# Kernel optimization log

Hardware: AMD Instinct MI355X
Metric: run time of the kernel (lower is better)

## Reference

```python
import jax, jax.numpy as jnp
import numpy as np

B, S, D, E, H, F, L, C = 32768, 5, 512, 256, 4, 2048, 2, 5  # batch, sensors, input_dim, embed_dim, heads, ffn, layers, classes
DH = E // H
EPS = 1e-5


def layer_norm(x, g, b):
    m = jnp.mean(x, axis=-1, keepdims=True)
    v = jnp.mean((x - m) ** 2, axis=-1, keepdims=True)
    return (x - m) * jax.lax.rsqrt(v + EPS) * g + b


def setup_inputs() -> dict:
    key = jax.random.key(0)
    ks = jax.random.split(key, 24)
    n = lambda k, shape: (jax.random.normal(k, shape, dtype=jnp.float32) * 0.02)
    return {
        "x": jax.random.normal(ks[0], (B, S, D), dtype=jnp.float32),
        "sensor_types": jax.random.randint(ks[1], (B, S), 0, 2, dtype=jnp.int32),
        "gps_w": n(ks[2], (E, D)), "gps_b": jnp.zeros((E,), jnp.float32),
        "ang_w": n(ks[3], (E, D)), "ang_b": jnp.zeros((E,), jnp.float32),
        "qkv_w": n(ks[4], (L, 3 * E, E)), "qkv_b": jnp.zeros((L, 3 * E), jnp.float32),
        "attn_ow": n(ks[5], (L, E, E)), "attn_ob": jnp.zeros((L, E), jnp.float32),
        "ln1_g": jnp.ones((L, E), jnp.float32), "ln1_b": jnp.zeros((L, E), jnp.float32),
        "ff1_w": n(ks[6], (L, F, E)), "ff1_b": jnp.zeros((L, F), jnp.float32),
        "ff2_w": n(ks[7], (L, E, F)), "ff2_b": jnp.zeros((L, E), jnp.float32),
        "ln2_g": jnp.ones((L, E), jnp.float32), "ln2_b": jnp.zeros((L, E), jnp.float32),
        "fc1_w": n(ks[8], (128, S * E)), "fc1_b": jnp.zeros((128,), jnp.float32),
        "fc2_w": n(ks[9], (64, 128)), "fc2_b": jnp.zeros((64,), jnp.float32),
        "out_w": n(ks[10], (C, 64)), "out_b": jnp.zeros((C,), jnp.float32),
    }


def reference(x, sensor_types, gps_w, gps_b, ang_w, ang_b, qkv_w, qkv_b,
              attn_ow, attn_ob, ln1_g, ln1_b, ff1_w, ff1_b, ff2_w, ff2_b,
              ln2_g, ln2_b, fc1_w, fc1_b, fc2_w, fc2_b, out_w, out_b):
    # Dual-expert routing: compute both branches, blend by mask (same math as masked scatter)
    is_gps = (sensor_types == 0)[..., None]  # [B,S,1]
    g = jax.nn.relu(jnp.einsum('bsd,ed->bse', x, gps_w) + gps_b)
    a = jax.nn.relu(jnp.einsum('bsd,ed->bse', x, ang_w) + ang_b)
    h = jnp.where(is_gps, g, a)  # [B,S,E]

    # TransformerEncoder (post-LN, ReLU FFN, dropout inactive at eval)
    for l in range(L):
        qkv = jnp.einsum('bse,fe->bsf', h, qkv_w[l]) + qkv_b[l]  # [B,S,3E]
        q, k, v = jnp.split(qkv, 3, axis=-1)
        q = q.reshape(B, S, H, DH); k = k.reshape(B, S, H, DH); v = v.reshape(B, S, H, DH)
        scores = jnp.einsum('bqhd,bkhd->bhqk', q, k) / jnp.sqrt(jnp.float32(DH))
        attn = jax.nn.softmax(scores, axis=-1)
        o = jnp.einsum('bhqk,bkhd->bqhd', attn, v).reshape(B, S, E)
        o = o @ attn_ow[l].T + attn_ob[l]
        h = layer_norm(h + o, ln1_g[l], ln1_b[l])
        ff = jax.nn.relu(h @ ff1_w[l].T + ff1_b[l]) @ ff2_w[l].T + ff2_b[l]
        h = layer_norm(h + ff, ln2_g[l], ln2_b[l])

    z = h.reshape(B, S * E)
    z = z @ fc1_w.T + fc1_b
    z = z @ fc2_w.T + fc2_b
    return z @ out_w.T + out_b
```

## Files before the change

kernel.cpp:

```cpp
#include <hip/hip_runtime.h>


#define N_TOK 163840
#define NBATCH 32768

typedef __attribute__((ext_vector_type(8))) short bfrag;
typedef __attribute__((ext_vector_type(4))) float f32x4;

__device__ __forceinline__ float bf2f(ushort u) {
  return __builtin_bit_cast(float, (uint)u << 16);
}
__device__ __forceinline__ ushort f2bf(float f) {
  uint u = __builtin_bit_cast(uint, f);
  return (ushort)((u + 0x7FFFu + ((u >> 16) & 1u)) >> 16);
}

__global__ __launch_bounds__(256) void cvt_kernel(const float* __restrict__ in,
                                                  ushort* __restrict__ out, int n4) {
  int i = blockIdx.x * 256 + threadIdx.x;
  if (i >= n4) return;
  float4 v = ((const float4*)in)[i];
  ushort4 o;
  o.x = f2bf(v.x); o.y = f2bf(v.y); o.z = f2bf(v.z); o.w = f2bf(v.w);
  ((ushort4*)out)[i] = o;
}

enum { EPI_F32 = 0, EPI_F32_RELU = 1, EPI_BF16 = 2, EPI_BF16_RELU = 3, EPI_SELECT = 4 };

template <int EPI>
__global__ __launch_bounds__(256) void gemm_bt(const ushort* __restrict__ A,
                                               const ushort* __restrict__ W,
                                               const float* __restrict__ bias,
                                               void* __restrict__ outp,
                                               int M, int K, int O,
                                               const float* __restrict__ gbuf,
                                               const int* __restrict__ stype,
                                               ushort* __restrict__ h16out) {
  __shared__ ushort As[128][32];
  __shared__ ushort Bs[128][32];
  const int tid = threadIdx.x;
  const int wave = tid >> 6, lane = tid & 63;
  const int bm = blockIdx.y, bn = blockIdx.x;
  const int wm = (wave & 1) << 6, wn = (wave >> 1) << 6;
  const int srow = tid >> 2;
  const int sq   = tid & 3;
  const int sc   = ((sq ^ ((srow >> 2) & 3))) << 3;
  const int scol = sq << 3;

  const ushort* Abase = A + (size_t)(bm * 128 + srow) * K + scol;
  const ushort* Wbase = W + (size_t)(bn * 128 + srow) * K + scol;

  f32x4 acc[4][4];
#pragma unroll
  for (int i = 0; i < 4; i++)
#pragma unroll
    for (int j = 0; j < 4; j++) acc[i][j] = {0.f, 0.f, 0.f, 0.f};

  const int fr = lane & 15;
  const int fq = lane >> 4;
  const int rc = (fq ^ ((fr >> 2) & 3)) << 3;

  uint4 a0 = *(const uint4*)(Abase);
  uint4 a1 = *(const uint4*)(Abase + (size_t)64 * K);
  uint4 b0 = *(const uint4*)(Wbase);
  uint4 b1 = *(const uint4*)(Wbase + (size_t)64 * K);

  for (int k0 = 0; k0 < K; k0 += 32) {
    *(uint4*)&As[srow][sc]      = a0;
    *(uint4*)&As[srow + 64][sc] = a1;
    *(uint4*)&Bs[srow][sc]      = b0;
    *(uint4*)&Bs[srow + 64][sc] = b1;
    __syncthreads();
    if (k0 + 32 < K) {
      a0 = *(const uint4*)(Abase + k0 + 32);
      a1 = *(const uint4*)(Abase + k0 + 32 + (size_t)64 * K);
      b0 = *(const uint4*)(Wbase + k0 + 32);
      b1 = *(const uint4*)(Wbase + k0 + 32 + (size_t)64 * K);
    }
    bfrag af[4], bf_[4];
#pragma unroll
    for (int i = 0; i < 4; i++) af[i] = *(const bfrag*)&As[wm + i * 16 + fr][rc];
#pragma unroll
    for (int j = 0; j < 4; j++) bf_[j] = *(const bfrag*)&Bs[wn + j * 16 + fr][rc];
#pragma unroll
    for (int i = 0; i < 4; i++)
#pragma unroll
      for (int j = 0; j < 4; j++)
        acc[i][j] = __builtin_amdgcn_mfma_f32_16x16x32_bf16(af[i], bf_[j], acc[i][j], 0, 0, 0);
    __syncthreads();
  }

  const int cr = fq << 2;
  const int cc = fr;
#pragma unroll
  for (int j = 0; j < 4; j++) {
    const int col = bn * 128 + wn + j * 16 + cc;
    const float bv = bias[col];
#pragma unroll
    for (int i = 0; i < 4; i++) {
      const int row = bm * 128 + wm + i * 16 + cr;
#pragma unroll
      for (int r = 0; r < 4; r++) {
        float v = acc[i][j][r] + bv;
        const size_t idx = (size_t)(row + r) * O + col;
        if (EPI != EPI_F32 && EPI != EPI_BF16) v = fmaxf(v, 0.f);
        if (EPI == EPI_SELECT) {
          if (stype[row + r] == 0) v = gbuf[idx];
          ((float*)outp)[idx] = v;
          h16out[idx] = f2bf(v);
        } else if (EPI == EPI_F32 || EPI == EPI_F32_RELU) {
          ((float*)outp)[idx] = v;
        } else {
          ((ushort*)outp)[idx] = f2bf(v);
        }
      }
    }
  }
}

__global__ __launch_bounds__(512) void gemm_lnres(const ushort* __restrict__ A,
                                                  const ushort* __restrict__ W,
                                                  const float* __restrict__ bias,
                                                  float* __restrict__ h32,
                                                  ushort* __restrict__ h16,
                                                  const float* __restrict__ g,
                                                  const float* __restrict__ b,
                                                  int K) {
  __shared__ ushort As[128][32];
  __shared__ ushort Bs[256][32];
  __shared__ float2 s_part[128][4];
  __shared__ float2 s_mr[128];
  const int tid = threadIdx.x;
  const int wave = tid >> 6, lane = tid & 63;
  const int bm = blockIdx.x;
  const int wm = (wave & 1) << 6, wn = (wave >> 1) << 6;

  const int srow = tid >> 2;
  const int sq   = tid & 3;
  const int sc   = ((sq ^ ((srow >> 2) & 3))) << 3;
  const int scol = sq << 3;
  const ushort* Ag = A + (size_t)(bm * 128 + srow) * K + scol;
  const ushort* Wg = W + (size_t)srow * K + scol;

  f32x4 acc[4][4];
#pragma unroll
  for (int i = 0; i < 4; i++)
#pragma unroll
    for (int j = 0; j < 4; j++) acc[i][j] = {0.f, 0.f, 0.f, 0.f};

  const int fr = lane & 15;
  const int fq = lane >> 4;
  const int rc = (fq ^ ((fr >> 2) & 3)) << 3;

  uint4 a0 = *(const uint4*)(Ag);
  uint4 b0 = *(const uint4*)(Wg);
  uint4 b1 = *(const uint4*)(Wg + (size_t)128 * K);

  for (int k0 = 0; k0 < K; k0 += 32) {
    *(uint4*)&As[srow][sc]       = a0;
    *(uint4*)&Bs[srow][sc]       = b0;
    *(uint4*)&Bs[srow + 128][sc] = b1;
    __syncthreads();
    if (k0 + 32 < K) {
      a0 = *(const uint4*)(Ag + k0 + 32);
      b0 = *(const uint4*)(Wg + k0 + 32);
      b1 = *(const uint4*)(Wg + k0 + 32 + (size_t)128 * K);
    }
    bfrag af[4], bf_[4];
#pragma unroll
    for (int i = 0; i < 4; i++) af[i] = *(const bfrag*)&As[wm + i * 16 + fr][rc];
#pragma unroll
    for (int j = 0; j < 4; j++) bf_[j] = *(const bfrag*)&Bs[wn + j * 16 + fr][rc];
#pragma unroll
    for (int i = 0; i < 4; i++)
#pragma unroll
      for (int j = 0; j < 4; j++)
        acc[i][j] = __builtin_amdgcn_mfma_f32_16x16x32_bf16(af[i], bf_[j], acc[i][j], 0, 0, 0);
    __syncthreads();
  }

  const int cr = fq << 2;
  const int cc = fr;
#pragma unroll
  for (int i = 0; i < 4; i++) {
#pragma unroll
    for (int r = 0; r < 4; r++) {
      const int row = wm + i * 16 + cr + r;
      const size_t grow = (size_t)(bm * 128 + row) * 256;
      float s = 0.f, sq2 = 0.f;
#pragma unroll
      for (int j = 0; j < 4; j++) {
        const int col = wn + j * 16 + cc;
        float u = acc[i][j][r] + bias[col] + h32[grow + col];
        acc[i][j][r] = u;
        s += u; sq2 += u * u;
      }
#pragma unroll
      for (int o = 1; o < 16; o <<= 1) { s += __shfl_xor(s, o); sq2 += __shfl_xor(sq2, o); }
      if ((lane & 15) == 0) s_part[row][wave >> 1] = {s, sq2};
    }
  }
  __syncthreads();
  if (tid < 128) {
    float2 p0 = s_part[tid][0], p1 = s_part[tid][1], p2 = s_part[tid][2], p3 = s_part[tid][3];
    float S = p0.x + p1.x + p2.x + p3.x;
    float SQ = p0.y + p1.y + p2.y + p3.y;
    float mean = S * 0.00390625f;
    float var = SQ * 0.00390625f - mean * mean;
    s_mr[tid] = {mean, rsqrtf(var + 1e-5f)};
  }
  __syncthreads();
#pragma unroll
  for (int i = 0; i < 4; i++) {
#pragma unroll
    for (int r = 0; r < 4; r++) {
      const int row = wm + i * 16 + cr + r;
      const float2 mr = s_mr[row];
      const size_t grow = (size_t)(bm * 128 + row) * 256;
#pragma unroll
      for (int j = 0; j < 4; j++) {
        const int col = wn + j * 16 + cc;
        float y = (acc[i][j][r] - mr.x) * mr.y * g[col] + b[col];
        h32[grow + col] = y;
        h16[grow + col] = f2bf(y);
      }
    }
  }
}

__global__ __launch_bounds__(256, 3) void ffn_fused(const ushort* __restrict__ h16in,
                                                    const ushort* __restrict__ W1,
                                                    const float* __restrict__ b1,
                                                    const ushort* __restrict__ W2,
                                                    const float* __restrict__ b2,
                                                    float* __restrict__ h32,
                                                    ushort* __restrict__ h16out,
                                                    const float* __restrict__ g,
                                                    const float* __restrict__ bb) {
  __shared__ ushort sh[64][264];
  __shared__ ushort smid[64][136];
  __shared__ float2 s_part[64][4];
  __shared__ float2 s_mr[64];
  const int tid = threadIdx.x;
  const int wave = tid >> 6, lane = tid & 63;
  const size_t tok0 = (size_t)blockIdx.x * 64;

  {
    const int r = tid >> 2, c0 = (tid & 3) << 6;
    const ushort* src = h16in + (tok0 + r) * 256 + c0;
#pragma unroll
    for (int u = 0; u < 8; u++)
      *(uint4*)&sh[r][c0 + u * 8] = *(const uint4*)(src + u * 8);
  }

  const int fr = lane & 15;
  const int fq = lane >> 4;
  const int cr = fq << 2;
  const int cc = fr;
  const int mq = wave << 5;
  const int oq = wave << 6;

  const ushort* w1p = W1 + (size_t)(mq + fr) * 256 + fq * 8;
  const ushort* w2p = W2 + (size_t)(oq + fr) * 2048 + fq * 8;

  f32x4 acc2[4][4];
#pragma unroll
  for (int i = 0; i < 4; i++)
#pragma unroll
    for (int j = 0; j < 4; j++) acc2[i][j] = {0.f, 0.f, 0.f, 0.f};

  bfrag nb1[2];
  nb1[0] = *(const bfrag*)(w1p);
  nb1[1] = *(const bfrag*)(w1p + 16 * 256);

  __syncthreads();

  for (int c = 0; c < 16; c++) {
    const size_t c1 = (size_t)c * 32768;
    f32x4 acc1[4][2];
#pragma unroll
    for (int i = 0; i < 4; i++)
#pragma unroll
      for (int j = 0; j < 2; j++) acc1[i][j] = {0.f, 0.f, 0.f, 0.f};
#pragma unroll
    for (int k = 0; k < 8; k++) {
      bfrag b1f[2];
      if (k == 0) { b1f[0] = nb1[0]; b1f[1] = nb1[1]; }
      else {
        b1f[0] = *(const bfrag*)(w1p + c1 + k * 32);
        b1f[1] = *(const bfrag*)(w1p + c1 + 16 * 256 + k * 32);
      }
      const int ko = k * 32 + fq * 8;
      bfrag af[4];
#pragma unroll
      for (int i = 0; i < 4; i++) af[i] = *(const bfrag*)&sh[i * 16 + fr][ko];
      __builtin_amdgcn_s_setprio(1);
#pragma unroll
      for (int i = 0; i < 4; i++)
#pragma unroll
        for (int j = 0; j < 2; j++)
          acc1[i][j] = __builtin_amdgcn_mfma_f32_16x16x32_bf16(af[i], b1f[j], acc1[i][j], 0, 0, 0);
      __builtin_amdgcn_s_setprio(0);
    }
    bfrag nb2[4];
#pragma unroll
    for (int j = 0; j < 4; j++)
      nb2[j] = *(const bfrag*)(w2p + (size_t)j * 32768 + c * 128);

    __syncthreads();
#pragma unroll
    for (int j = 0; j < 2; j++) {
      const float bv = b1[c * 128 + mq + j * 16 + cc];
#pragma unroll
      for (int i = 0; i < 4; i++)
#pragma unroll
        for (int r = 0; r < 4; r++) {
          float v = fmaxf(acc1[i][j][r] + bv, 0.f);
          smid[i * 16 + cr + r][mq + j * 16 + cc] = f2bf(v);
        }
    }
    __syncthreads();
#pragma unroll
    for (int k = 0; k < 4; k++) {
      bfrag b2f[4];
      if (k == 0) {
        b2f[0] = nb2[0]; b2f[1] = nb2[1]; b2f[2] = nb2[2]; b2f[3] = nb2[3];
        const size_t cn = (size_t)((c + 1) & 15) * 32768;
        nb1[0] = *(const bfrag*)(w1p + cn);
        nb1[1] = *(const bfrag*)(w1p + cn + 16 * 256);
      } else {
#pragma unroll
        for (int j = 0; j < 4; j++)
          b2f[j] = *(const bfrag*)(w2p + (size_t)j * 32768 + c * 128 + k * 32);
      }
      const int ko = k * 32 + fq * 8;
      bfrag af[4];
#pragma unroll
      for (int i = 0; i < 4; i++) af[i] = *(const bfrag*)&smid[i * 16 + fr][ko];
      __builtin_amdgcn_s_setprio(1);
#pragma unroll
      for (int i = 0; i < 4; i++)
#pragma unroll
        for (int j = 0; j < 4; j++)
          acc2[i][j] = __builtin_amdgcn_mfma_f32_16x16x32_bf16(af[i], b2f[j], acc2[i][j], 0, 0, 0);
      __builtin_amdgcn_s_setprio(0);
    }
  }

#pragma unroll
  for (int i = 0; i < 4; i++) {
#pragma unroll
    for (int r = 0; r < 4; r++) {
      const int row = i * 16 + cr + r;
      const size_t grow = (tok0 + row) * 256;
      float s = 0.f, sq2 = 0.f;
#pragma unroll
      for (int j = 0; j < 4; j++) {
        const int col = oq + j * 16 + cc;
        float u = acc2[i][j][r] + b2[col] + h32[grow + col];
        acc2[i][j][r] = u;
        s += u; sq2 += u * u;
      }
#pragma unroll
      for (int o = 1; o < 16; o <<= 1) { s += __shfl_xor(s, o); sq2 += __shfl_xor(sq2, o); }
      if ((lane & 15) == 0) s_part[row][wave] = {s, sq2};
    }
  }
  __syncthreads();
  if (tid < 64) {
    float2 p0 = s_part[tid][0], p1 = s_part[tid][1], p2 = s_part[tid][2], p3 = s_part[tid][3];
    float S = p0.x + p1.x + p2.x + p3.x;
    float SQ = p0.y + p1.y + p2.y + p3.y;
    float mean = S * 0.00390625f;
    float var = SQ * 0.00390625f - mean * mean;
    s_mr[tid] = {mean, rsqrtf(var + 1e-5f)};
  }
  __syncthreads();
#pragma unroll
  for (int i = 0; i < 4; i++) {
#pragma unroll
    for (int r = 0; r < 4; r++) {
      const int row = i * 16 + cr + r;
      const float2 mr = s_mr[row];
      const size_t grow = (tok0 + row) * 256;
#pragma unroll
      for (int j = 0; j < 4; j++) {
        const int col = oq + j * 16 + cc;
        float y = (acc2[i][j][r] - mr.x) * mr.y * g[col] + bb[col];
        h32[grow + col] = y;
        h16out[grow + col] = f2bf(y);
      }
    }
  }
}

__global__ __launch_bounds__(256) void attn_kernel(const ushort* __restrict__ qkv,
                                                   ushort* __restrict__ o16) {
  __shared__ ushort s_qkv[8 * 5 * 768];
  __shared__ float s_att[8 * 4 * 25];
  const int tid = threadIdx.x;
  const size_t gbase = (size_t)blockIdx.x * (8 * 5 * 768);
#pragma unroll
  for (int t = 0; t < 15; t++) {
    int i = tid + t * 256;
    *(uint4*)&s_qkv[i * 8] = *(const uint4*)(qkv + gbase + (size_t)i * 8);
  }
  __syncthreads();
  for (int idx = tid; idx < 800; idx += 256) {
    int b = idx / 100, r = idx - b * 100;
    int h = r / 25, ij = r - h * 25;
    int i = ij / 5, j = ij - i * 5;
    const ushort* qp = &s_qkv[(b * 5 + i) * 768 + h * 64];
    const ushort* kp = &s_qkv[(b * 5 + j) * 768 + 256 + h * 64];
    float s = 0.f;
#pragma unroll
    for (int d = 0; d < 64; d += 2) {
      uint qw = *(const uint*)&qp[d];
      uint kw = *(const uint*)&kp[d];
      s += bf2f((ushort)(qw & 0xffffu)) * bf2f((ushort)(kw & 0xffffu));
      s += bf2f((ushort)(qw >> 16)) * bf2f((ushort)(kw >> 16));
    }
    s_att[idx] = s * 0.125f;
  }
  __syncthreads();
  if (tid < 160) {
    float* sp = &s_att[tid * 5];
    float m = fmaxf(fmaxf(fmaxf(sp[0], sp[1]), fmaxf(sp[2], sp[3])), sp[4]);
    float e0 = __expf(sp[0] - m), e1 = __expf(sp[1] - m), e2 = __expf(sp[2] - m);
    float e3 = __expf(sp[3] - m), e4 = __expf(sp[4] - m);
    float inv = 1.f / (e0 + e1 + e2 + e3 + e4);
    sp[0] = e0 * inv; sp[1] = e1 * inv; sp[2] = e2 * inv; sp[3] = e3 * inv; sp[4] = e4 * inv;
  }
  __syncthreads();
  const size_t obase = (size_t)blockIdx.x * (8 * 5 * 256);
#pragma unroll
  for (int t = 0; t < 40; t++) {
    int idx = t * 256 + tid;
    int d = idx & 63;
    int rest = idx >> 6;
    int h = rest & 3; rest >>= 2;
    int i = rest % 5, b = rest / 5;
    const float* ap = &s_att[(b * 4 + h) * 25 + i * 5];
    const ushort* vp = &s_qkv[(b * 5) * 768 + 512 + h * 64 + d];
    float o = 0.f;
#pragma unroll
    for (int j = 0; j < 5; j++) o += ap[j] * bf2f(vp[j * 768]);
    o16[obase + (size_t)((b * 5 + i) * 256 + h * 64 + d)] = f2bf(o);
  }
}

__global__ __launch_bounds__(256) void head2_kernel(const float* __restrict__ z1,
                                                    const float* __restrict__ fc2w,
                                                    const float* __restrict__ fc2b,
                                                    const float* __restrict__ outw,
                                                    const float* __restrict__ outb,
                                                    float* __restrict__ out) {
  __shared__ float s_z2[4][64];
  const int wave = threadIdx.x >> 6, lane = threadIdx.x & 63;
  const int b = blockIdx.x * 4 + wave;
  const float* z = z1 + (size_t)b * 128;
  float acc = fc2b[lane];
#pragma unroll 8
  for (int k = 0; k < 128; k++) acc += z[k] * fc2w[lane * 128 + k];
  s_z2[wave][lane] = acc;
  __syncthreads();
  if (lane < 5) {
    const float* zz = s_z2[wave];
    float o = outb[lane];
#pragma unroll 8
    for (int k = 0; k < 64; k++) o += zz[k] * outw[lane * 64 + k];
    out[(size_t)b * 5 + lane] = o;
  }
}

extern "C" void kernel_launch(void* const* d_in, const int* in_sizes, int n_in,
                              void* d_out, int out_size, void* d_ws, size_t ws_size,
                              hipStream_t stream) {
  const float* x       = (const float*)d_in[0];
  const int*   stype   = (const int*)d_in[1];
  const float* gps_w   = (const float*)d_in[2];
  const float* gps_b   = (const float*)d_in[3];
  const float* ang_w   = (const float*)d_in[4];
  const float* ang_b   = (const float*)d_in[5];
  const float* qkv_w   = (const float*)d_in[6];
  const float* qkv_b   = (const float*)d_in[7];
  const float* attn_ow = (const float*)d_in[8];
  const float* attn_ob = (const float*)d_in[9];
  const float* ln1_g   = (const float*)d_in[10];
  const float* ln1_b   = (const float*)d_in[11];
  const float* ff1_w   = (const float*)d_in[12];
  const float* ff1_b   = (const float*)d_in[13];
  const float* ff2_w   = (const float*)d_in[14];
  const float* ff2_b   = (const float*)d_in[15];
  const float* ln2_g   = (const float*)d_in[16];
  const float* ln2_b   = (const float*)d_in[17];
  const float* fc1_w   = (const float*)d_in[18];
  const float* fc1_b   = (const float*)d_in[19];
  const float* fc2_w   = (const float*)d_in[20];
  const float* fc2_b   = (const float*)d_in[21];
  const float* out_w   = (const float*)d_in[22];
  const float* out_b   = (const float*)d_in[23];

  char* ws = (char*)d_ws;
  const size_t NEED = 763363328ull;
  if (ws_size < NEED) return;

  ushort* w_gps  = (ushort*)ws;
  ushort* w_ang  = w_gps + 131072;
  ushort* w_qkv  = w_ang + 131072;
  ushort* w_attn = w_qkv + 393216;
  ushort* w_ff1  = w_attn + 131072;
  ushort* w_ff2  = w_ff1 + 1048576;
  ushort* w_fc1  = w_ff2 + 1048576;

  ushort* R16 = (ushort*)(ws + (size_t)(8u << 20));
  ushort* h16 = (ushort*)(ws + 8388608ull + 251658240ull);
  float*  h32 = (float*)(ws + 8388608ull + 251658240ull + 83886080ull);
  float*  t32 = (float*)(ws + 8388608ull + 251658240ull + 83886080ull + 167772160ull);
  ushort* o16 = (ushort*)(ws + 8388608ull + 251658240ull + 83886080ull + 335544320ull);

  auto cvt = [&](const float* src, ushort* dst, int n4) {
    cvt_kernel<<<(n4 + 255) / 256, 256, 0, stream>>>(src, dst, n4);
  };
  cvt(gps_w, w_gps, 32768);
  cvt(ang_w, w_ang, 32768);
  cvt(qkv_w, w_qkv, 98304);
  cvt(attn_ow, w_attn, 32768);
  cvt(ff1_w, w_ff1, 262144);
  cvt(ff2_w, w_ff2, 262144);
  cvt(fc1_w, w_fc1, 40960);
  cvt(x, R16, 20971520);

  gemm_bt<EPI_F32_RELU><<<dim3(2, 1280), 256, 0, stream>>>(
      R16, w_gps, gps_b, t32, N_TOK, 512, 256, nullptr, nullptr, nullptr);
  gemm_bt<EPI_SELECT><<<dim3(2, 1280), 256, 0, stream>>>(
      R16, w_ang, ang_b, h32, N_TOK, 512, 256, t32, stype, h16);

  for (int l = 0; l < 2; l++) {
    gemm_bt<EPI_BF16><<<dim3(6, 1280), 256, 0, stream>>>(
        h16, w_qkv + l * 196608, qkv_b + l * 768, R16, N_TOK, 256, 768,
        nullptr, nullptr, nullptr);
    attn_kernel<<<4096, 256, 0, stream>>>(R16, o16);
    gemm_lnres<<<1280, 512, 0, stream>>>(o16, w_attn + l * 65536, attn_ob + l * 256,
                                         h32, h16, ln1_g + l * 256, ln1_b + l * 256, 256);
    ffn_fused<<<2560, 256, 0, stream>>>(h16, w_ff1 + l * 524288, ff1_b + l * 2048,
                                        w_ff2 + l * 524288, ff2_b + l * 256,
                                        h32, h16, ln2_g + l * 256, ln2_b + l * 256);
  }

  gemm_bt<EPI_F32><<<dim3(1, 256), 256, 0, stream>>>(
      h16, w_fc1, fc1_b, t32, NBATCH, 1280, 128, nullptr, nullptr, nullptr);
  head2_kernel<<<8192, 256, 0, stream>>>(t32, fc2_w, fc2_b, out_w, out_b, (float*)d_out);
}
```

Before: 3.391 ms.

## Bulk-load FFN weight fragments per chunk and drop setprio hints in ffn_fused

```diff
diff --git a/kernel.cpp b/kernel.cpp
--- a/kernel.cpp
+++ b/kernel.cpp
@@ -228,7 +228,7 @@
   }
 }
 
-__global__ __launch_bounds__(256, 3) void ffn_fused(const ushort* __restrict__ h16in,
+__global__ __launch_bounds__(256, 2) void ffn_fused(const ushort* __restrict__ h16in,
                                                     const ushort* __restrict__ W1,
                                                     const float* __restrict__ b1,
                                                     const ushort* __restrict__ W2,
@@ -269,14 +269,20 @@
 #pragma unroll
     for (int j = 0; j < 4; j++) acc2[i][j] = {0.f, 0.f, 0.f, 0.f};
 
-  bfrag nb1[2];
-  nb1[0] = *(const bfrag*)(w1p);
-  nb1[1] = *(const bfrag*)(w1p + 16 * 256);
-
   __syncthreads();
 
   for (int c = 0; c < 16; c++) {
     const size_t c1 = (size_t)c * 32768;
+
+    bfrag w1f[8][2];
+#pragma unroll
+    for (int k = 0; k < 8; k++) {
+      w1f[k][0] = *(const bfrag*)(w1p + c1 + k * 32);
+      w1f[k][1] = *(const bfrag*)(w1p + c1 + 16 * 256 + k * 32);
+    }
+    const float bv0 = b1[c * 128 + mq + cc];
+    const float bv1 = b1[c * 128 + mq + 16 + cc];
+
     f32x4 acc1[4][2];
 #pragma unroll
     for (int i = 0; i < 4; i++)
@@ -284,66 +290,47 @@
       for (int j = 0; j < 2; j++) acc1[i][j] = {0.f, 0.f, 0.f, 0.f};
 #pragma unroll
     for (int k = 0; k < 8; k++) {
-      bfrag b1f[2];
-      if (k == 0) { b1f[0] = nb1[0]; b1f[1] = nb1[1]; }
-      else {
-        b1f[0] = *(const bfrag*)(w1p + c1 + k * 32);
-        b1f[1] = *(const bfrag*)(w1p + c1 + 16 * 256 + k * 32);
-      }
       const int ko = k * 32 + fq * 8;
       bfrag af[4];
 #pragma unroll
       for (int i = 0; i < 4; i++) af[i] = *(const bfrag*)&sh[i * 16 + fr][ko];
-      __builtin_amdgcn_s_setprio(1);
 #pragma unroll
       for (int i = 0; i < 4; i++)
 #pragma unroll
         for (int j = 0; j < 2; j++)
-          acc1[i][j] = __builtin_amdgcn_mfma_f32_16x16x32_bf16(af[i], b1f[j], acc1[i][j], 0, 0, 0);
-      __builtin_amdgcn_s_setprio(0);
-    }
-    bfrag nb2[4];
-#pragma unroll
-    for (int j = 0; j < 4; j++)
-      nb2[j] = *(const bfrag*)(w2p + (size_t)j * 32768 + c * 128);
+          acc1[i][j] = __builtin_amdgcn_mfma_f32_16x16x32_bf16(af[i], w1f[k][j], acc1[i][j], 0, 0, 0);
+    }
+
+    bfrag w2f[4][4];
+#pragma unroll
+    for (int k = 0; k < 4; k++)
+#pragma unroll
+      for (int j = 0; j < 4; j++)
+        w2f[k][j] = *(const bfrag*)(w2p + (size_t)j * 32768 + c * 128 + k * 32);
 
     __syncthreads();
 #pragma unroll
-    for (int j = 0; j < 2; j++) {
-      const float bv = b1[c * 128 + mq + j * 16 + cc];
-#pragma unroll
-      for (int i = 0; i < 4; i++)
-#pragma unroll
-        for (int r = 0; r < 4; r++) {
-          float v = fmaxf(acc1[i][j][r] + bv, 0.f);
-          smid[i * 16 + cr + r][mq + j * 16 + cc] = f2bf(v);
-        }
-    }
+    for (int i = 0; i < 4; i++)
+#pragma unroll
+      for (int r = 0; r < 4; r++) {
+        float v0 = fmaxf(acc1[i][0][r] + bv0, 0.f);
+        float v1 = fmaxf(acc1[i][1][r] + bv1, 0.f);
+        smid[i * 16 + cr + r][mq + cc]      = f2bf(v0);
+        smid[i * 16 + cr + r][mq + 16 + cc] = f2bf(v1);
+      }
     __syncthreads();
+
 #pragma unroll
     for (int k = 0; k < 4; k++) {
-      bfrag b2f[4];
-      if (k == 0) {
-        b2f[0] = nb2[0]; b2f[1] = nb2[1]; b2f[2] = nb2[2]; b2f[3] = nb2[3];
-        const size_t cn = (size_t)((c + 1) & 15) * 32768;
-        nb1[0] = *(const bfrag*)(w1p + cn);
-        nb1[1] = *(const bfrag*)(w1p + cn + 16 * 256);
-      } else {
-#pragma unroll
-        for (int j = 0; j < 4; j++)
-          b2f[j] = *(const bfrag*)(w2p + (size_t)j * 32768 + c * 128 + k * 32);
-      }
       const int ko = k * 32 + fq * 8;
       bfrag af[4];
 #pragma unroll
       for (int i = 0; i < 4; i++) af[i] = *(const bfrag*)&smid[i * 16 + fr][ko];
-      __builtin_amdgcn_s_setprio(1);
 #pragma unroll
       for (int i = 0; i < 4; i++)
 #pragma unroll
         for (int j = 0; j < 4; j++)
-          acc2[i][j] = __builtin_amdgcn_mfma_f32_16x16x32_bf16(af[i], b2f[j], acc2[i][j], 0, 0, 0);
-      __builtin_amdgcn_s_setprio(0);
+          acc2[i][j] = __builtin_amdgcn_mfma_f32_16x16x32_bf16(af[i], w2f[k][j], acc2[i][j], 0, 0, 0);
     }
   }
 
```

Result: faster. 3.135 ms (-7.5%).
